# Kernel tuning notes

Measured on AMD Instinct MI355X. Metric: run time of the kernel, lower is better.

The kernel has to match this reference:

```python
import jax, jax.numpy as jnp
import numpy as np

D_MODEL, NUM_HEADS, D_HEAD = 1024, 16, 64
B, T = 2, 2048


def setup_inputs() -> dict:
    key = jax.random.key(0)
    ks = jax.random.split(key, 9)
    s_in = 1.0 / np.sqrt(D_MODEL)
    s_proj = 1.0 / np.sqrt(NUM_HEADS * D_HEAD)
    x = jax.random.normal(ks[0], (B, T, D_MODEL), dtype=jnp.float32)
    # stacked per-head projection weights (nn.Linear: y = x @ W.T + b -> store as [H, C, d_head])
    Wq = jax.random.uniform(ks[1], (NUM_HEADS, D_MODEL, D_HEAD), jnp.float32, -s_in, s_in)
    Wk = jax.random.uniform(ks[2], (NUM_HEADS, D_MODEL, D_HEAD), jnp.float32, -s_in, s_in)
    Wv = jax.random.uniform(ks[3], (NUM_HEADS, D_MODEL, D_HEAD), jnp.float32, -s_in, s_in)
    bq = jax.random.uniform(ks[4], (NUM_HEADS, D_HEAD), jnp.float32, -s_in, s_in)
    bk = jax.random.uniform(ks[5], (NUM_HEADS, D_HEAD), jnp.float32, -s_in, s_in)
    bv = jax.random.uniform(ks[6], (NUM_HEADS, D_HEAD), jnp.float32, -s_in, s_in)
    Wo = jax.random.uniform(ks[7], (NUM_HEADS * D_HEAD, D_MODEL), jnp.float32, -s_proj, s_proj)
    bo = jax.random.uniform(ks[8], (D_MODEL,), jnp.float32, -s_proj, s_proj)
    return {"x": x, "Wq": Wq, "Wk": Wk, "Wv": Wv, "bq": bq, "bk": bk, "bv": bv, "Wo": Wo, "bo": bo}


def reference(x, Wq, Wk, Wv, bq, bk, bv, Wo, bo):
    Bsz, Tlen, C = x.shape
    # per-head projections, vectorized over heads: [B, H, T, d_head]
    q = jnp.einsum('btc,hcd->bhtd', x, Wq) + bq[None, :, None, :]
    k = jnp.einsum('btc,hcd->bhtd', x, Wk) + bk[None, :, None, :]
    v = jnp.einsum('btc,hcd->bhtd', x, Wv) + bv[None, :, None, :]
    # NOTE: source scales by sqrt(C) = sqrt(d_model), not sqrt(d_head); no causal mask
    scores = jnp.einsum('bhtd,bhsd->bhts', q, k) / jnp.sqrt(jnp.asarray(C, x.dtype))
    attn = jax.nn.softmax(scores, axis=-1)
    out = jnp.einsum('bhts,bhsd->bhtd', attn, v)  # [B, H, T, d_head]
    # concat heads along feature dim: [B, T, H*d_head]
    out = jnp.transpose(out, (0, 2, 1, 3)).reshape(Bsz, Tlen, -1)
    return out @ Wo + bo
```

## Files before the change

kernel.cpp:

```cpp
#include <hip/hip_runtime.h>

typedef __bf16 bf16;
typedef __bf16 bf16x4 __attribute__((ext_vector_type(4)));
typedef __bf16 bf16x8 __attribute__((ext_vector_type(8)));
typedef float  f32x4  __attribute__((ext_vector_type(4)));

#define T_SEQ  2048
#define NHEAD  16
#define DHEAD  64
#define DMODEL 1024
#define MTOT   4096
#define L2E    1.4426950408889634f

static __device__ __forceinline__ f32x4 mfma16(bf16x8 a, bf16x8 b, f32x4 c) {
    return __builtin_amdgcn_mfma_f32_16x16x32_bf16(a, b, c, 0, 0, 0);
}

__global__ __launch_bounds__(256) void prep(
    const float* __restrict__ x,  bf16* __restrict__ xbf,
    const float* __restrict__ Wq, const float* __restrict__ Wk,
    const float* __restrict__ Wv, bf16* __restrict__ wt,
    const float* __restrict__ Wo, bf16* __restrict__ wot)
{
    __shared__ float t[64][68];
    const int bid = blockIdx.x, tid = threadIdx.x;

    if (bid < 2048) {
        const int i = bid * 256 + tid;
        const float4 a = ((const float4*)x)[i * 2];
        const float4 b = ((const float4*)x)[i * 2 + 1];
        bf16x8 v;
        v[0] = (bf16)a.x; v[1] = (bf16)a.y; v[2] = (bf16)a.z; v[3] = (bf16)a.w;
        v[4] = (bf16)b.x; v[5] = (bf16)b.y; v[6] = (bf16)b.z; v[7] = (bf16)b.w;
        ((bf16x8*)xbf)[i] = v;
        return;
    }

    const float* in; bf16* out;
    int R, Cc; long ib, ob; int r0, c0;
    if (bid < 2816) {
        int b2 = bid - 2048;
        int w = b2 >> 8, rem = b2 & 255;
        int rt = rem & 15, head = rem >> 4;
        in  = (w == 0 ? Wq : w == 1 ? Wk : Wv);
        out = wt + (size_t)w * 1024 * 1024;
        R = 1024; Cc = 64;
        ib = (long)head * 65536; ob = (long)head * 65536;
        r0 = rt * 64; c0 = 0;
    } else {
        int b3 = bid - 2816;
        in = Wo; out = wot;
        R = 1024; Cc = 1024;
        ib = 0; ob = 0;
        r0 = (b3 & 15) * 64; c0 = (b3 >> 4) * 64;
    }

#pragma unroll
    for (int i = 0; i < 4; ++i) {
        int idx = i * 256 + tid;
        int row = idx >> 4, cb = (idx & 15) * 4;
        float4 v = *(const float4*)&in[ib + (long)(r0 + row) * Cc + c0 + cb];
        t[row][cb + 0] = v.x; t[row][cb + 1] = v.y;
        t[row][cb + 2] = v.z; t[row][cb + 3] = v.w;
    }
    __syncthreads();
#pragma unroll
    for (int i = 0; i < 2; ++i) {
        int idx = i * 256 + tid;
        int row = idx >> 3, cb = (idx & 7) * 8;
        bf16x8 v;
#pragma unroll
        for (int j = 0; j < 8; ++j) v[j] = (bf16)t[cb + j][row];
        *(bf16x8*)&out[ob + (long)(c0 + row) * R + r0 + cb] = v;
    }
}

__global__ __launch_bounds__(256) void qkv_gemm(
    const bf16* __restrict__ x, const bf16* __restrict__ wt,
    const float* __restrict__ bq, const float* __restrict__ bk,
    const float* __restrict__ bv,
    bf16* __restrict__ qws, bf16* __restrict__ kws, bf16* __restrict__ vtws)
{
    __shared__ __align__(16) bf16 xs[128][72];
    __shared__ __align__(16) bf16 wsh[3][64][72];

    const int m0 = blockIdx.x * 128;
    const int h  = blockIdx.y;
    const int tid = threadIdx.x, wid = tid >> 6, lane = tid & 63;
    const int lr = lane & 15, lg = lane >> 4;

    const bf16* wbase[3];
#pragma unroll
    for (int w = 0; w < 3; ++w)
        wbase[w] = wt + ((size_t)(w * NHEAD + h)) * DHEAD * DMODEL;

    f32x4 acc[3][2][4];
#pragma unroll
    for (int w = 0; w < 3; ++w)
#pragma unroll
        for (int mi = 0; mi < 2; ++mi)
#pragma unroll
            for (int nt = 0; nt < 4; ++nt) acc[w][mi][nt] = (f32x4)0.0f;

    bf16x8 xr[4], wr[3][2];
#pragma unroll
    for (int i = 0; i < 4; ++i) {
        int idx = i * 256 + tid;
        int row = idx >> 3, cb = (idx & 7) * 8;
        xr[i] = *(const bf16x8*)&x[(size_t)(m0 + row) * DMODEL + cb];
    }
#pragma unroll
    for (int w = 0; w < 3; ++w)
#pragma unroll
        for (int i = 0; i < 2; ++i) {
            int idx = i * 256 + tid;
            int row = idx >> 3, cb = (idx & 7) * 8;
            wr[w][i] = *(const bf16x8*)&wbase[w][(size_t)row * DMODEL + cb];
        }

    for (int kt = 0; kt < 16; ++kt) {
        __syncthreads();
#pragma unroll
        for (int i = 0; i < 4; ++i) {
            int idx = i * 256 + tid;
            int row = idx >> 3, cb = (idx & 7) * 8;
            *(bf16x8*)&xs[row][cb] = xr[i];
        }
#pragma unroll
        for (int w = 0; w < 3; ++w)
#pragma unroll
            for (int i = 0; i < 2; ++i) {
                int idx = i * 256 + tid;
                int row = idx >> 3, cb = (idx & 7) * 8;
                *(bf16x8*)&wsh[w][row][cb] = wr[w][i];
            }
        __syncthreads();

        if (kt < 15) {
            const int kofs = (kt + 1) * 64;
#pragma unroll
            for (int i = 0; i < 4; ++i) {
                int idx = i * 256 + tid;
                int row = idx >> 3, cb = (idx & 7) * 8;
                xr[i] = *(const bf16x8*)&x[(size_t)(m0 + row) * DMODEL + kofs + cb];
            }
#pragma unroll
            for (int w = 0; w < 3; ++w)
#pragma unroll
                for (int i = 0; i < 2; ++i) {
                    int idx = i * 256 + tid;
                    int row = idx >> 3, cb = (idx & 7) * 8;
                    wr[w][i] = *(const bf16x8*)&wbase[w][(size_t)row * DMODEL + kofs + cb];
                }
        }

        bf16x8 af[2][2];
#pragma unroll
        for (int mi = 0; mi < 2; ++mi)
#pragma unroll
            for (int ks = 0; ks < 2; ++ks)
                af[mi][ks] = *(const bf16x8*)&xs[wid * 32 + mi * 16 + lr][ks * 32 + lg * 8];

#pragma unroll
        for (int w = 0; w < 3; ++w)
#pragma unroll
            for (int nt = 0; nt < 4; ++nt)
#pragma unroll
                for (int ks = 0; ks < 2; ++ks) {
                    bf16x8 bfr = *(const bf16x8*)&wsh[w][nt * 16 + lr][ks * 32 + lg * 8];
#pragma unroll
                    for (int mi = 0; mi < 2; ++mi)
                        acc[w][mi][nt] = mfma16(af[mi][ks], bfr, acc[w][mi][nt]);
                }
    }

    const float* bias[3] = { bq + h * DHEAD, bk + h * DHEAD, bv + h * DHEAD };
#pragma unroll
    for (int w = 0; w < 3; ++w)
#pragma unroll
        for (int nt = 0; nt < 4; ++nt) {
            int d = nt * 16 + lr;
            float bs = bias[w][d];
#pragma unroll
            for (int mi = 0; mi < 2; ++mi)
#pragma unroll
                for (int j = 0; j < 4; ++j) {
                    int mrow = m0 + wid * 32 + mi * 16 + lg * 4 + j;
                    int b = mrow >> 11, t = mrow & 2047;
                    float val = acc[w][mi][nt][j] + bs;
                    size_t bh = (size_t)b * NHEAD + h;
                    if (w == 0)
                        qws[(bh * T_SEQ + t) * DHEAD + d] = (bf16)val;
                    else if (w == 1)
                        kws[(bh * T_SEQ + t) * DHEAD + d] = (bf16)val;
                    else
                        vtws[(bh * DHEAD + d) * T_SEQ + t] = (bf16)val;
                }
        }
}

template<int S, bool PARTIAL>
__global__ __launch_bounds__(512, 4) void attn_split(
    const bf16* __restrict__ qws, const bf16* __restrict__ kws,
    const bf16* __restrict__ vtws,
    bf16* __restrict__ po, float* __restrict__ pml, bf16* __restrict__ aws)
{
    __shared__ __align__(16) bf16 kls[2][64][72];
    __shared__ __align__(16) bf16 vls[2][64][72];

    const int id = blockIdx.x;
    const int w  = (id & 7) * (32 * S) + (id >> 3);
    const int bh = w / (8 * S);
    const int rem = w - bh * (8 * S);
    const int qt = rem / S;
    const int sidx = rem - qt * S;
    const int t0 = (sidx * 32) / S, t1 = ((sidx + 1) * 32) / S;

    const int b = bh >> 4, h = bh & 15;
    const bf16* Q  = qws  + (size_t)bh * T_SEQ * DHEAD;
    const bf16* K  = kws  + (size_t)bh * T_SEQ * DHEAD;
    const bf16* Vt = vtws + (size_t)bh * DHEAD * T_SEQ;

    const int tid = threadIdx.x, wid = tid >> 6, lane = tid & 63;
    const int lr = lane & 15, lg = lane >> 4;

    const int srow = tid >> 3, scb = (tid & 7) * 8;
    const int sl = tid & 7;
    const int vcol = 32 * (sl >> 2) + 4 * (sl & 3);

    bf16x8 onesf;
#pragma unroll
    for (int j = 0; j < 8; ++j) onesf[j] = (bf16)1.0f;

    int q0[2];
    bf16x8 qf[2][2];
#pragma unroll
    for (int g = 0; g < 2; ++g) {
        q0[g] = qt * 256 + g * 128 + wid * 16;
#pragma unroll
        for (int ks = 0; ks < 2; ++ks) {
            bf16x8 v = *(const bf16x8*)&Q[(size_t)(q0[g] + lr) * DHEAD + ks * 32 + lg * 8];
#pragma unroll
            for (int j = 0; j < 8; ++j) v[j] = (bf16)((float)v[j] * 0.03125f);
            qf[g][ks] = v;
        }
    }

    f32x4 o[2][4], lsum[2];
#pragma unroll
    for (int g = 0; g < 2; ++g) {
#pragma unroll
        for (int nt = 0; nt < 4; ++nt) o[g][nt] = (f32x4)0.0f;
        lsum[g] = (f32x4)0.0f;
    }
    float mrun[2] = { -1e30f, -1e30f };
    float m2c[2]  = { -1e30f * L2E, -1e30f * L2E };

    bf16x8 kr;
    bf16x4 va, vb;
    kr = *(const bf16x8*)&K[(size_t)(t0 * 64 + srow) * DHEAD + scb];
    va = *(const bf16x4*)&Vt[(size_t)srow * T_SEQ + t0 * 64 + vcol];
    vb = *(const bf16x4*)&Vt[(size_t)srow * T_SEQ + t0 * 64 + vcol + 16];
    *(bf16x8*)&kls[0][srow][scb] = kr;
    *(bf16x8*)&vls[0][srow][scb] = __builtin_shufflevector(va, vb, 0, 1, 2, 3, 4, 5, 6, 7);

    int cur = 0;
    for (int t = t0; t < t1; ++t) {
        __syncthreads();

        const bool more = (t + 1) < t1;
        if (more) {
            int kvn = (t + 1) * 64;
            kr = *(const bf16x8*)&K[(size_t)(kvn + srow) * DHEAD + scb];
            va = *(const bf16x4*)&Vt[(size_t)srow * T_SEQ + kvn + vcol];
            vb = *(const bf16x4*)&Vt[(size_t)srow * T_SEQ + kvn + vcol + 16];
        }

        f32x4 s[2][4];
        __builtin_amdgcn_s_setprio(1);
#pragma unroll
        for (int nt = 0; nt < 4; ++nt) {
            bf16x8 k0 = *(const bf16x8*)&kls[cur][nt * 16 + lr][0 + lg * 8];
            bf16x8 k1 = *(const bf16x8*)&kls[cur][nt * 16 + lr][32 + lg * 8];
#pragma unroll
            for (int g = 0; g < 2; ++g) {
                s[g][nt] = mfma16(k0, qf[g][0], (f32x4)0.0f);
                s[g][nt] = mfma16(k1, qf[g][1], s[g][nt]);
            }
        }
        __builtin_amdgcn_s_setprio(0);

        bf16x8 pf[2][2];
#pragma unroll
        for (int g = 0; g < 2; ++g) {
            float vm0 = fmaxf(fmaxf(s[g][0][0], s[g][0][1]), fmaxf(s[g][0][2], s[g][0][3]));
            float vm1 = fmaxf(fmaxf(s[g][1][0], s[g][1][1]), fmaxf(s[g][1][2], s[g][1][3]));
            float vm2 = fmaxf(fmaxf(s[g][2][0], s[g][2][1]), fmaxf(s[g][2][2], s[g][2][3]));
            float vm3 = fmaxf(fmaxf(s[g][3][0], s[g][3][1]), fmaxf(s[g][3][2], s[g][3][3]));
            float vm = fmaxf(fmaxf(vm0, vm1), fmaxf(vm2, vm3));

            const bool skip = __all(vm <= mrun[g] + 8.0f);
            if (!skip) {
                float vmr = fmaxf(vm, __shfl_xor(vm, 16));
                vmr = fmaxf(vmr, __shfl_xor(vmr, 32));
                float mnew = fmaxf(mrun[g], vmr);
                float alpha = __builtin_amdgcn_exp2f((mrun[g] - mnew) * L2E);
                mrun[g] = mnew;
                m2c[g] = mnew * L2E;
                float ab[4];
#pragma unroll
                for (int j = 0; j < 4; ++j) ab[j] = __shfl(alpha, lg * 4 + j);
#pragma unroll
                for (int j = 0; j < 4; ++j) lsum[g][j] *= ab[j];
#pragma unroll
                for (int nt = 0; nt < 4; ++nt)
#pragma unroll
                    for (int j = 0; j < 4; ++j) o[g][nt][j] *= ab[j];
            }

            const float m2 = m2c[g];
            float p[4][4];
#pragma unroll
            for (int nt = 0; nt < 4; ++nt)
#pragma unroll
                for (int j = 0; j < 4; ++j)
                    p[nt][j] = __builtin_amdgcn_exp2f(fmaf(s[g][nt][j], L2E, -m2));

#pragma unroll
            for (int ks = 0; ks < 2; ++ks) {
                bf16x8 pk;
#pragma unroll
                for (int j = 0; j < 4; ++j) {
                    pk[j]     = (bf16)p[2 * ks][j];
                    pk[j + 4] = (bf16)p[2 * ks + 1][j];
                }
                pf[g][ks] = pk;
            }
        }

        __builtin_amdgcn_s_setprio(1);
#pragma unroll
        for (int ks = 0; ks < 2; ++ks) {
#pragma unroll
            for (int g = 0; g < 2; ++g)
                lsum[g] = mfma16(pf[g][ks], onesf, lsum[g]);
#pragma unroll
            for (int nt = 0; nt < 4; ++nt) {
                bf16x8 vf = *(const bf16x8*)&vls[cur][nt * 16 + lr][ks * 32 + lg * 8];
#pragma unroll
                for (int g = 0; g < 2; ++g)
                    o[g][nt] = mfma16(pf[g][ks], vf, o[g][nt]);
            }
        }
        __builtin_amdgcn_s_setprio(0);

        if (more) {
            *(bf16x8*)&kls[cur ^ 1][srow][scb] = kr;
            *(bf16x8*)&vls[cur ^ 1][srow][scb] =
                __builtin_shufflevector(va, vb, 0, 1, 2, 3, 4, 5, 6, 7);
        }
        cur ^= 1;
    }

#pragma unroll
    for (int g = 0; g < 2; ++g) {
        float linv[4];
#pragma unroll
        for (int j = 0; j < 4; ++j) linv[j] = 1.0f / lsum[g][j];

        if (PARTIAL) {
            const size_t pbase = (size_t)(sidx * 32 + bh) * T_SEQ * DHEAD;
#pragma unroll
            for (int nt = 0; nt < 4; ++nt) {
                int dcol = nt * 16 + lr;
#pragma unroll
                for (int j = 0; j < 4; ++j) {
                    int tq = q0[g] + lg * 4 + j;
                    po[pbase + (size_t)tq * DHEAD + dcol] = (bf16)(o[g][nt][j] * linv[j]);
                }
            }
            {
                int js = lr & 3;
                float wv = lsum[g][0];
                wv = (js == 1) ? lsum[g][1] : wv;
                wv = (js == 2) ? lsum[g][2] : wv;
                wv = (js == 3) ? lsum[g][3] : wv;
                float lrow_q = __shfl(wv, 16 * (lr >> 2) + (lr & 3));
                if (lg == 0) {
                    size_t mlidx = ((size_t)(sidx * 32 + bh) * T_SEQ + (q0[g] + lr)) * 2;
                    pml[mlidx]     = mrun[g];
                    pml[mlidx + 1] = lrow_q;
                }
            }
        } else {
            const size_t obase = ((size_t)b * T_SEQ) * DMODEL + (size_t)h * DHEAD;
#pragma unroll
            for (int nt = 0; nt < 4; ++nt) {
                int dcol = nt * 16 + lr;
#pragma unroll
                for (int j = 0; j < 4; ++j) {
                    int tq = q0[g] + lg * 4 + j;
                    aws[obase + (size_t)tq * DMODEL + dcol] = (bf16)(o[g][nt][j] * linv[j]);
                }
            }
        }
    }
}

template<int S>
__global__ __launch_bounds__(256) void attn_combine(
    const bf16* __restrict__ po, const float* __restrict__ pml,
    bf16* __restrict__ aws)
{
    const int g = blockIdx.x * 256 + threadIdx.x;
    const int r = g >> 3, dblk = g & 7;
    const int bh = r >> 11, tq = r & 2047;

    float ms[S], ls[S];
    float m = -1e30f;
#pragma unroll
    for (int s = 0; s < S; ++s) {
        float2 v = ((const float2*)pml)[(size_t)(s * 32 + bh) * T_SEQ + tq];
        ms[s] = v.x; ls[s] = v.y;
        m = fmaxf(m, ms[s]);
    }
    float L = 0.f, wgt[S];
#pragma unroll
    for (int s = 0; s < S; ++s) {
        wgt[s] = ls[s] * __builtin_amdgcn_exp2f((ms[s] - m) * L2E);
        L += wgt[s];
    }
    float inv = 1.0f / L;

    float acc[8];
#pragma unroll
    for (int j = 0; j < 8; ++j) acc[j] = 0.f;
#pragma unroll
    for (int s = 0; s < S; ++s) {
        bf16x8 ov = *(const bf16x8*)&po[((size_t)(s * 32 + bh) * T_SEQ + tq) * DHEAD + dblk * 8];
        float c = wgt[s] * inv;
#pragma unroll
        for (int j = 0; j < 8; ++j) acc[j] = fmaf(c, (float)ov[j], acc[j]);
    }
    bf16x8 out;
#pragma unroll
    for (int j = 0; j < 8; ++j) out[j] = (bf16)acc[j];

    const int b = bh >> 4, h = bh & 15;
    *(bf16x8*)&aws[((size_t)(b * T_SEQ + tq)) * DMODEL + h * DHEAD + dblk * 8] = out;
}

__global__ __launch_bounds__(256) void out_gemm(
    const bf16* __restrict__ a, const bf16* __restrict__ wot,
    const float* __restrict__ bo, float* __restrict__ out)
{
    __shared__ __align__(16) bf16 as[64][72];
    __shared__ __align__(16) bf16 wsh[128][72];

    const int m0 = blockIdx.x * 64, n0 = blockIdx.y * 128;
    const int tid = threadIdx.x, wid = tid >> 6, lane = tid & 63;
    const int lr = lane & 15, lg = lane >> 4;

    f32x4 acc[8];
#pragma unroll
    for (int nt = 0; nt < 8; ++nt) acc[nt] = (f32x4)0.0f;

    bf16x8 ar[2], wr[4];
#pragma unroll
    for (int i = 0; i < 2; ++i) {
        int idx = i * 256 + tid;
        int row = idx >> 3, cb = (idx & 7) * 8;
        ar[i] = *(const bf16x8*)&a[(size_t)(m0 + row) * DMODEL + cb];
    }
#pragma unroll
    for (int i = 0; i < 4; ++i) {
        int idx = i * 256 + tid;
        int row = idx >> 3, cb = (idx & 7) * 8;
        wr[i] = *(const bf16x8*)&wot[(size_t)(n0 + row) * DMODEL + cb];
    }

    for (int kt = 0; kt < 16; ++kt) {
        __syncthreads();
#pragma unroll
        for (int i = 0; i < 2; ++i) {
            int idx = i * 256 + tid;
            int row = idx >> 3, cb = (idx & 7) * 8;
            *(bf16x8*)&as[row][cb] = ar[i];
        }
#pragma unroll
        for (int i = 0; i < 4; ++i) {
            int idx = i * 256 + tid;
            int row = idx >> 3, cb = (idx & 7) * 8;
            *(bf16x8*)&wsh[row][cb] = wr[i];
        }
        __syncthreads();

        if (kt < 15) {
            const int kofs = (kt + 1) * 64;
#pragma unroll
            for (int i = 0; i < 2; ++i) {
                int idx = i * 256 + tid;
                int row = idx >> 3, cb = (idx & 7) * 8;
                ar[i] = *(const bf16x8*)&a[(size_t)(m0 + row) * DMODEL + kofs + cb];
            }
#pragma unroll
            for (int i = 0; i < 4; ++i) {
                int idx = i * 256 + tid;
                int row = idx >> 3, cb = (idx & 7) * 8;
                wr[i] = *(const bf16x8*)&wot[(size_t)(n0 + row) * DMODEL + kofs + cb];
            }
        }

        bf16x8 af[2];
#pragma unroll
        for (int ks = 0; ks < 2; ++ks)
            af[ks] = *(const bf16x8*)&as[wid * 16 + lr][ks * 32 + lg * 8];

#pragma unroll
        for (int nt = 0; nt < 8; ++nt)
#pragma unroll
            for (int ks = 0; ks < 2; ++ks) {
                bf16x8 bfr = *(const bf16x8*)&wsh[nt * 16 + lr][ks * 32 + lg * 8];
                acc[nt] = mfma16(af[ks], bfr, acc[nt]);
            }
    }

#pragma unroll
    for (int nt = 0; nt < 8; ++nt) {
        int n = n0 + nt * 16 + lr;
        float bs = bo[n];
#pragma unroll
        for (int j = 0; j < 4; ++j) {
            int m = m0 + wid * 16 + lg * 4 + j;
            out[(size_t)m * DMODEL + n] = acc[nt][j] + bs;
        }
    }
}

extern "C" void kernel_launch(void* const* d_in, const int* in_sizes, int n_in,
                              void* d_out, int out_size, void* d_ws, size_t ws_size,
                              hipStream_t stream)
{
    const float* x  = (const float*)d_in[0];
    const float* Wq = (const float*)d_in[1];
    const float* Wk = (const float*)d_in[2];
    const float* Wv = (const float*)d_in[3];
    const float* bq = (const float*)d_in[4];
    const float* bk = (const float*)d_in[5];
    const float* bv = (const float*)d_in[6];
    const float* Wo = (const float*)d_in[7];
    const float* bo = (const float*)d_in[8];
    float* out = (float*)d_out;

    const size_t M1 = (size_t)1024 * 1024;
    bf16* ws   = (bf16*)d_ws;
    bf16* xbf  = ws;
    bf16* qws  = ws + 4 * M1;
    bf16* kws  = qws + 4 * M1;
    bf16* vtws = kws + 4 * M1;
    bf16* wt   = vtws + 4 * M1;
    bf16* wot  = wt + 3 * M1;
    bf16* aws  = xbf;
    bf16* po   = wot + 1 * M1;

    const size_t BASE = 20 * M1 * 2;
    const size_t PER  = 4 * M1 * 2 + (size_t)65536 * 2 * 4;

    dim3 tb(256);
    prep<<<dim3(3072), tb, 0, stream>>>(x, xbf, Wq, Wk, Wv, wt, Wo, wot);
    qkv_gemm<<<dim3(MTOT / 128, NHEAD), tb, 0, stream>>>(xbf, wt, bq, bk, bv, qws, kws, vtws);

    if (ws_size >= BASE + 2 * PER) {
        float* pml = (float*)(po + 2 * 4 * M1);
        attn_split<2, true><<<dim3(512), dim3(512), 0, stream>>>(qws, kws, vtws, po, pml, aws);
        attn_combine<2><<<dim3(2048), tb, 0, stream>>>(po, pml, aws);
    } else {
        attn_split<1, false><<<dim3(256), dim3(512), 0, stream>>>(qws, kws, vtws, po, nullptr, aws);
    }

    out_gemm<<<dim3(MTOT / 64, DMODEL / 128), tb, 0, stream>>>(aws, wot, bo, out);
}
```

Before: 115.9 us.

## Fuse split-KV attention combine into output projection GEMM A-tile load

Removes the separate attn_combine kernel and merges the two split-KV partial outputs inside out_gemm while loading the A operand, using each partial's max and sum to weight it. This saves one launch plus the write and reread of the combined attention buffer. In exchange, every one of the 8 N-column blocks recomputes the combine and reads both partials and their m/l values, which multiplies global reads of the partials and adds exp and divide work in the GEMM load path.

```diff
diff --git a/kernel.cpp b/kernel.cpp
--- a/kernel.cpp
+++ b/kernel.cpp
@@ -407,52 +407,12 @@
     }
 }
 
-template<int S>
-__global__ __launch_bounds__(256) void attn_combine(
+template<bool FUSED>
+__global__ __launch_bounds__(256) void out_gemm(
+    const bf16* __restrict__ a,
     const bf16* __restrict__ po, const float* __restrict__ pml,
-    bf16* __restrict__ aws)
-{
-    const int g = blockIdx.x * 256 + threadIdx.x;
-    const int r = g >> 3, dblk = g & 7;
-    const int bh = r >> 11, tq = r & 2047;
-
-    float ms[S], ls[S];
-    float m = -1e30f;
-#pragma unroll
-    for (int s = 0; s < S; ++s) {
-        float2 v = ((const float2*)pml)[(size_t)(s * 32 + bh) * T_SEQ + tq];
-        ms[s] = v.x; ls[s] = v.y;
-        m = fmaxf(m, ms[s]);
-    }
-    float L = 0.f, wgt[S];
-#pragma unroll
-    for (int s = 0; s < S; ++s) {
-        wgt[s] = ls[s] * __builtin_amdgcn_exp2f((ms[s] - m) * L2E);
-        L += wgt[s];
-    }
-    float inv = 1.0f / L;
-
-    float acc[8];
-#pragma unroll
-    for (int j = 0; j < 8; ++j) acc[j] = 0.f;
-#pragma unroll
-    for (int s = 0; s < S; ++s) {
-        bf16x8 ov = *(const bf16x8*)&po[((size_t)(s * 32 + bh) * T_SEQ + tq) * DHEAD + dblk * 8];
-        float c = wgt[s] * inv;
-#pragma unroll
-        for (int j = 0; j < 8; ++j) acc[j] = fmaf(c, (float)ov[j], acc[j]);
-    }
-    bf16x8 out;
-#pragma unroll
-    for (int j = 0; j < 8; ++j) out[j] = (bf16)acc[j];
-
-    const int b = bh >> 4, h = bh & 15;
-    *(bf16x8*)&aws[((size_t)(b * T_SEQ + tq)) * DMODEL + h * DHEAD + dblk * 8] = out;
-}
-
-__global__ __launch_bounds__(256) void out_gemm(
-    const bf16* __restrict__ a, const bf16* __restrict__ wot,
-    const float* __restrict__ bo, float* __restrict__ out)
+    const bf16* __restrict__ wot, const float* __restrict__ bo,
+    float* __restrict__ out)
 {
     __shared__ __align__(16) bf16 as[64][72];
     __shared__ __align__(16) bf16 wsh[128][72];
@@ -465,12 +425,28 @@
 #pragma unroll
     for (int nt = 0; nt < 8; ++nt) acc[nt] = (f32x4)0.0f;
 
-    bf16x8 ar[2], wr[4];
+    bf16x8 ar[2], p0r[2], p1r[2], wr[4];
+    float w0r[2], w1r[2];
+
 #pragma unroll
     for (int i = 0; i < 2; ++i) {
         int idx = i * 256 + tid;
         int row = idx >> 3, cb = (idx & 7) * 8;
-        ar[i] = *(const bf16x8*)&a[(size_t)(m0 + row) * DMODEL + cb];
+        if (!FUSED) {
+            ar[i] = *(const bf16x8*)&a[(size_t)(m0 + row) * DMODEL + cb];
+        } else {
+            int m = m0 + row, b = m >> 11, t = m & 2047;
+            int bh = b * NHEAD + 0;
+            p0r[i] = *(const bf16x8*)&po[((size_t)bh * T_SEQ + t) * DHEAD + cb];
+            p1r[i] = *(const bf16x8*)&po[((size_t)(32 + bh) * T_SEQ + t) * DHEAD + cb];
+            float2 ml0 = ((const float2*)pml)[(size_t)bh * T_SEQ + t];
+            float2 ml1 = ((const float2*)pml)[(size_t)(32 + bh) * T_SEQ + t];
+            float mm = fmaxf(ml0.x, ml1.x);
+            float u0 = ml0.y * __builtin_amdgcn_exp2f((ml0.x - mm) * L2E);
+            float u1 = ml1.y * __builtin_amdgcn_exp2f((ml1.x - mm) * L2E);
+            float inv = 1.0f / (u0 + u1);
+            w0r[i] = u0 * inv; w1r[i] = u1 * inv;
+        }
     }
 #pragma unroll
     for (int i = 0; i < 4; ++i) {
@@ -485,7 +461,15 @@
         for (int i = 0; i < 2; ++i) {
             int idx = i * 256 + tid;
             int row = idx >> 3, cb = (idx & 7) * 8;
-            *(bf16x8*)&as[row][cb] = ar[i];
+            if (!FUSED) {
+                *(bf16x8*)&as[row][cb] = ar[i];
+            } else {
+                bf16x8 v;
+#pragma unroll
+                for (int j = 0; j < 8; ++j)
+                    v[j] = (bf16)(w0r[i] * (float)p0r[i][j] + w1r[i] * (float)p1r[i][j]);
+                *(bf16x8*)&as[row][cb] = v;
+            }
         }
 #pragma unroll
         for (int i = 0; i < 4; ++i) {
@@ -497,11 +481,26 @@
 
         if (kt < 15) {
             const int kofs = (kt + 1) * 64;
+            const int hn = kt + 1;
 #pragma unroll
             for (int i = 0; i < 2; ++i) {
                 int idx = i * 256 + tid;
                 int row = idx >> 3, cb = (idx & 7) * 8;
-                ar[i] = *(const bf16x8*)&a[(size_t)(m0 + row) * DMODEL + kofs + cb];
+                if (!FUSED) {
+                    ar[i] = *(const bf16x8*)&a[(size_t)(m0 + row) * DMODEL + kofs + cb];
+                } else {
+                    int m = m0 + row, b = m >> 11, t = m & 2047;
+                    int bh = b * NHEAD + hn;
+                    p0r[i] = *(const bf16x8*)&po[((size_t)bh * T_SEQ + t) * DHEAD + cb];
+                    p1r[i] = *(const bf16x8*)&po[((size_t)(32 + bh) * T_SEQ + t) * DHEAD + cb];
+                    float2 ml0 = ((const float2*)pml)[(size_t)bh * T_SEQ + t];
+                    float2 ml1 = ((const float2*)pml)[(size_t)(32 + bh) * T_SEQ + t];
+                    float mm = fmaxf(ml0.x, ml1.x);
+                    float u0 = ml0.y * __builtin_amdgcn_exp2f((ml0.x - mm) * L2E);
+                    float u1 = ml1.y * __builtin_amdgcn_exp2f((ml1.x - mm) * L2E);
+                    float inv = 1.0f / (u0 + u1);
+                    w0r[i] = u0 * inv; w1r[i] = u1 * inv;
+                }
             }
 #pragma unroll
             for (int i = 0; i < 4; ++i) {
@@ -573,10 +572,11 @@
     if (ws_size >= BASE + 2 * PER) {
         float* pml = (float*)(po + 2 * 4 * M1);
         attn_split<2, true><<<dim3(512), dim3(512), 0, stream>>>(qws, kws, vtws, po, pml, aws);
-        attn_combine<2><<<dim3(2048), tb, 0, stream>>>(po, pml, aws);
+        out_gemm<true><<<dim3(MTOT / 64, DMODEL / 128), tb, 0, stream>>>(
+            aws, po, pml, wot, bo, out);
     } else {
         attn_split<1, false><<<dim3(256), dim3(512), 0, stream>>>(qws, kws, vtws, po, nullptr, aws);
-    }
-
-    out_gemm<<<dim3(MTOT / 64, DMODEL / 128), tb, 0, stream>>>(aws, wot, bo, out);
+        out_gemm<false><<<dim3(MTOT / 64, DMODEL / 128), tb, 0, stream>>>(
+            aws, nullptr, nullptr, wot, bo, out);
+    }
 }
```

Result: slower. 120.3 us (+3.8%).
